# Optimization experiments

Measured on AMD Instinct MI355X. Metric: run time of the kernel, lower is better.

The kernel has to match this reference:

```python
import jax, jax.numpy as jnp
import numpy as np

K = 16          # neighbors per point
POINTNUM = 2048 # opt.pointnum
B, N = 8, 2048


def _knn_concat(x, k):
    """x: [B,N,C] -> [B,N,k,2C] = concat(center, k-nearest neighbor feats)."""
    sq = jnp.sum(x * x, axis=-1)                                   # [B,N]
    d2 = sq[:, :, None] + sq[:, None, :] - 2.0 * jnp.einsum('bnc,bmc->bnm', x, x)
    _, idx = jax.lax.top_k(-d2, k)                                 # [B,N,k]
    nbr = jax.vmap(lambda xb, ib: xb[ib])(x, idx)                  # [B,N,k,C]
    ctr = jnp.broadcast_to(x[:, :, None, :], nbr.shape)
    return jnp.concatenate([ctr, nbr], axis=-1)


def _lin(x, w, b):
    return x @ w + b


lrelu = jax.nn.leaky_relu  # default negative_slope=0.01 matches nn.LeakyReLU()


def setup_inputs() -> dict:
    key = jax.random.key(0)
    ks = jax.random.split(key, 20)

    def w(k_, fi, fo):
        return jax.random.normal(k_, (fi, fo), jnp.float32) / np.sqrt(fi)

    inp = {
        'x': jax.random.normal(ks[0], (B, N, 3), jnp.float32),
        'h1w1': w(ks[1], 6, 16),   'h1b1': jnp.zeros((16,), jnp.float32),
        'h1w2': w(ks[2], 16, 64),  'h1b2': jnp.zeros((64,), jnp.float32),
        'h1w3': w(ks[3], 64, 32),  'h1b3': jnp.zeros((32,), jnp.float32),
        'h2w1': w(ks[4], 64, 256), 'h2b1': jnp.zeros((256,), jnp.float32),
        'h2w2': w(ks[5], 256, 128),'h2b2': jnp.zeros((128,), jnp.float32),
        'h3w1': w(ks[6], 256, 128),'h3b1': jnp.zeros((128,), jnp.float32),
        'fc1w': w(ks[7], 128, 128),'fc1b': jnp.zeros((128,), jnp.float32),
        'fc2w': w(ks[8], 128, 128),'fc2b': jnp.zeros((128,), jnp.float32),
        'fc3w': w(ks[9], 128, POINTNUM * 3), 'fc3b': jnp.zeros((POINTNUM * 3,), jnp.float32),
    }
    return inp


def reference(x, h1w1, h1b1, h1w2, h1b2, h1w3, h1b3,
              h2w1, h2b1, h2w2, h2b2, h3w1, h3b1,
              fc1w, fc1b, fc2w, fc2b, fc3w, fc3b):
    # block 1: knn-concat [B,N,K,6] -> MLP(6,16,64,32) -> sum over K
    x1 = _knn_concat(x, K)
    h = lrelu(_lin(x1, h1w1, h1b1))
    h = lrelu(_lin(h, h1w2, h1b2))
    h = lrelu(_lin(h, h1w3, h1b3))
    x2 = jnp.sum(h, axis=2)                    # [B,N,32]
    # block 2: [B,N,K,64] -> MLP(64,256,128) -> sum over K
    x2 = _knn_concat(x2, K)
    h = lrelu(_lin(x2, h2w1, h2b1))
    h = lrelu(_lin(h, h2w2, h2b2))
    x3 = jnp.sum(h, axis=2)                    # [B,N,128]
    # block 3: [B,N,K,256] -> MLP(256,128) -> sum over K
    x3 = _knn_concat(x3, K)
    h = lrelu(_lin(x3, h3w1, h3b1))
    x4 = jnp.sum(h, axis=2)                    # [B,N,128]
    # global max pool over points
    x5 = jnp.max(x4, axis=1)                   # [B,128]
    x6 = lrelu(_lin(x5, fc1w, fc1b))
    x7 = lrelu(_lin(x6, fc2w, fc2b))
    x8 = _lin(x7, fc3w, fc3b)                  # [B, POINTNUM*3]
    return x8.reshape(x8.shape[0], POINTNUM, 3)
```

## Files before the change

kernel.cpp:

```cpp
#include <hip/hip_runtime.h>

#define KNB 16
#define BSZ 8
#define NPT 2048

typedef __attribute__((ext_vector_type(8))) short bf16x8;
typedef __attribute__((ext_vector_type(4))) float f32x4;

__device__ __forceinline__ float lrelu(float x) { return x >= 0.f ? x : 0.01f * x; }

__device__ __forceinline__ unsigned short bf16rne(float f) {
    union { float f; unsigned int u; } v; v.f = f;
    return (unsigned short)((v.u + 0x7FFFu + ((v.u >> 16) & 1u)) >> 16);
}

__device__ __forceinline__ float packkey(float d, int idx) {
    union { float f; unsigned int u; } v; v.f = d;
    v.u = (v.u & 0xFFFFF800u) | (unsigned int)idx;
    return v.f;
}

__device__ __forceinline__ void ceA(float& a, float& b) {
    const float lo = fminf(a, b), hi = fmaxf(a, b);
    a = lo; b = hi;
}

__device__ __forceinline__ void bsort16(float* c) {
#pragma unroll
    for (int k = 2; k <= 16; k <<= 1) {
#pragma unroll
        for (int j = k >> 1; j > 0; j >>= 1) {
#pragma unroll
            for (int i = 0; i < 16; ++i) {
                const int l = i ^ j;
                if (l > i) {
                    if ((i & k) == 0) ceA(c[i], c[l]);
                    else              ceA(c[l], c[i]);
                }
            }
        }
    }
}

__device__ __forceinline__ void merge16(float* L, const float* C) {
#pragma unroll
    for (int i = 0; i < 16; ++i) L[i] = fminf(L[i], C[15 - i]);
#pragma unroll
    for (int j = 8; j > 0; j >>= 1) {
#pragma unroll
        for (int i = 0; i < 16; ++i) {
            const int l = i ^ j;
            if (l > i) ceA(L[i], L[l]);
        }
    }
}

__device__ __forceinline__ void st16(float* dst, const float* L) {
#pragma unroll
    for (int c = 0; c < 4; ++c)
        *(f32x4*)(dst + c * 4) = (f32x4){L[c * 4], L[c * 4 + 1], L[c * 4 + 2], L[c * 4 + 3]};
}

__device__ __forceinline__ void ld16(float* L, const float* src) {
#pragma unroll
    for (int c = 0; c < 4; ++c) {
        const f32x4 v = *(const f32x4*)(src + c * 4);
        L[c * 4] = v[0]; L[c * 4 + 1] = v[1]; L[c * 4 + 2] = v[2]; L[c * 4 + 3] = v[3];
    }
}

__device__ __forceinline__ void xwave_merge_out(float (*sS)[20], int w, int lane,
                                                float* L, float* outp) {
    st16(sS[w * 64 + lane], L);
    __syncthreads();
    if ((w & 1) == 0) {
        float C[16];
        ld16(C, sS[(w + 1) * 64 + lane]);
        merge16(L, C);
        if (w == 2) st16(sS[2 * 64 + lane], L);
    }
    __syncthreads();
    if (w == 0) {
        float C[16];
        ld16(C, sS[2 * 64 + lane]);
        merge16(L, C);
        st16(outp, L);
    }
}

__global__ void wprep_all_kernel(const float* __restrict__ h2w1, unsigned short* __restrict__ w1t,
                                 const float* __restrict__ h2w2, unsigned short* __restrict__ w2t,
                                 const float* __restrict__ h3w1, unsigned short* __restrict__ w3t,
                                 const float* __restrict__ w1, const float* __restrict__ w2,
                                 const float* __restrict__ w3,
                                 unsigned short* __restrict__ w1a, unsigned short* __restrict__ w2a,
                                 unsigned short* __restrict__ w3a) {
    const int bid = blockIdx.x, tid = threadIdx.x;
    if (bid < 64) {
        int i = bid * 256 + tid;
        int k = i >> 8, n = i & 255;
        w1t[n * 64 + k] = bf16rne(h2w1[i]);
    } else if (bid < 192) {
        int i = (bid - 64) * 256 + tid;
        int k = i >> 7, n = i & 127;
        w2t[n * 256 + k] = bf16rne(h2w2[i]);
    } else if (bid < 320) {
        int i = (bid - 192) * 256 + tid;
        int k = i >> 7, n = i & 127;
        w3t[n * 256 + k] = bf16rne(h3w1[i]);
    } else {
        int i = (bid - 320) * 256 + tid;
        if (i < 512) {
            int n = i >> 5, k = i & 31;
            w1a[i] = (k < 6) ? bf16rne(w1[k * 16 + n]) : (unsigned short)0;
        } else if (i < 2560) {
            int j = i - 512, n = j >> 5, k = j & 31;
            w2a[j] = (k < 16) ? bf16rne(w2[k * 64 + n]) : (unsigned short)0;
        } else if (i < 4608) {
            int j = i - 2560, n = j >> 6, k = j & 63;
            w3a[j] = bf16rne(w3[k * 32 + n]);
        }
    }
}

template<int C>
__global__ void norms_kernel(const float* __restrict__ feat, float* __restrict__ out) {
    int gid = blockIdx.x * blockDim.x + threadIdx.x;
    if (gid < BSZ * NPT) {
        const float* p = feat + (size_t)gid * C;
        float s = 0.f;
#pragma unroll
        for (int c = 0; c < C; ++c) s = fmaf(p[c], p[c], s);
        out[gid] = s;
    }
}

__global__ void norms16q_kernel(const unsigned short* __restrict__ feat, float* __restrict__ out) {
    const int gid = blockIdx.x * 256 + threadIdx.x;
    const int q = gid >> 2, prt = gid & 3;
    const unsigned short* p = feat + (size_t)q * 128 + prt * 32;
    float s = 0.f;
#pragma unroll
    for (int c8 = 0; c8 < 4; ++c8) {
        const bf16x8 v = *(const bf16x8*)(p + c8 * 8);
#pragma unroll
        for (int j = 0; j < 8; ++j) {
            union { unsigned int u; float f; } t;
            t.u = ((unsigned int)(unsigned short)v[j]) << 16;
            s = fmaf(t.f, t.f, s);
        }
    }
    s += __shfl_xor(s, 1);
    s += __shfl_xor(s, 2);
    if (prt == 0) out[q] = s;
}

template<int JS>
__launch_bounds__(256, 3)
__global__ void knn3_kernel(const float* __restrict__ feat,
                            const float* __restrict__ norms,
                            float* __restrict__ cand) {
    constexpr int JL = NPT / JS;
    constexpr int JP = JL / 4;
    const int b = blockIdx.z, js = blockIdx.y, i0 = blockIdx.x * 64;
    const int t = threadIdx.x, w = t >> 6, lane = t & 63;
    const float* fb = feat + (size_t)b * NPT * 3;
    const float* nb = norms + (size_t)b * NPT;

    __shared__ __align__(16) float sS[256][20];

    float q0, q1, q2;
    { const float* qp = fb + (size_t)(i0 + lane) * 3; q0 = qp[0]; q1 = qp[1]; q2 = qp[2]; }

    float L[16];
#pragma unroll
    for (int u = 0; u < 16; ++u) L[u] = 3e38f;

    const int jbeg = js * JL + w * JP;
#pragma unroll 1
    for (int j0 = jbeg; j0 < jbeg + JP; j0 += 16) {
        float C[16];
#pragma unroll
        for (int u = 0; u < 16; ++u) {
            const int j = j0 + u;
            const float* pp = fb + (size_t)j * 3;
            C[u] = packkey(fmaf(-2.f, fmaf(q0, pp[0], fmaf(q1, pp[1], q2 * pp[2])), nb[j]), j);
        }
        bsort16(C);
        merge16(L, C);
    }
    float* o = cand + (((size_t)b * NPT + i0 + lane) * JS + js) * 16;
    xwave_merge_out(sS, w, lane, L, o);
}

template<int C, int JS>
__launch_bounds__(256, 3)
__global__ void knn_mfma_kernel(const unsigned short* __restrict__ fb16,
                                const float* __restrict__ norms,
                                float* __restrict__ cand) {
    constexpr int JL = NPT / JS;
    constexpr int KS = C / 32;
    const int b    = blockIdx.z;
    const int js   = blockIdx.y;
    const int i0   = blockIdx.x * 64;
    const int t    = threadIdx.x;
    const int w    = t >> 6;
    const int lane = t & 63;
    const int l15  = lane & 15;
    const int quad = lane >> 4;
    const unsigned short* fbb = fb16 + (size_t)b * NPT * C;
    const float* nb = norms + (size_t)b * NPT;

    __shared__ __align__(16) float sS[256][20];

    bf16x8 afr[KS * 4];
#pragma unroll
    for (int ks = 0; ks < KS; ++ks)
#pragma unroll
        for (int mi = 0; mi < 4; ++mi)
            afr[ks * 4 + mi] = *(const bf16x8*)(fbb + (size_t)(i0 + mi * 16 + l15) * C + ks * 32 + quad * 8);

    float L[16];
#pragma unroll
    for (int u = 0; u < 16; ++u) L[u] = 3e38f;

    const int jbeg = js * JL;
#pragma unroll 1
    for (int j0 = jbeg; j0 < jbeg + JL; j0 += 64) {
        f32x4 acc[4];
#pragma unroll
        for (int mi = 0; mi < 4; ++mi) acc[mi] = (f32x4){0.f, 0.f, 0.f, 0.f};
        const unsigned short* prow = fbb + (size_t)(j0 + w * 16 + l15) * C + quad * 8;
#pragma unroll
        for (int ks = 0; ks < KS; ++ks) {
            const bf16x8 bfr = *(const bf16x8*)(prow + ks * 32);
#pragma unroll
            for (int mi = 0; mi < 4; ++mi)
                acc[mi] = __builtin_amdgcn_mfma_f32_16x16x32_bf16(afr[ks * 4 + mi], bfr, acc[mi], 0, 0, 0);
        }
        const float nv  = nb[j0 + w * 16 + l15];
        const int  cidx = j0 + w * 16 + l15;
#pragma unroll
        for (int mi = 0; mi < 4; ++mi)
#pragma unroll
            for (int r = 0; r < 4; ++r)
                sS[w * 64 + mi * 16 + quad * 4 + r][l15] = packkey(fmaf(-2.f, acc[mi][r], nv), cidx);
        float Cb[16];
        ld16(Cb, sS[w * 64 + lane]);
        bsort16(Cb);
        merge16(L, Cb);
    }

    float* o = cand + (((size_t)b * NPT + i0 + lane) * JS + js) * 16;
    xwave_merge_out(sS, w, lane, L, o);
}

template<int JS>
__launch_bounds__(64)
__global__ void knn_merge_kernel(const float* __restrict__ cand, int* __restrict__ knn_out) {
    const int q = blockIdx.x * 64 + threadIdx.x;
    const float* pd = cand + (size_t)q * JS * 16;
    float L[16];
    ld16(L, pd);
#pragma unroll
    for (int s = 1; s < JS; ++s) {
        float C[16];
        ld16(C, pd + s * 16);
        merge16(L, C);
    }
    int* o = knn_out + (size_t)q * KNB;
#pragma unroll
    for (int u = 0; u < 16; ++u) {
        union { float f; unsigned int v; } z; z.f = L[u];
        o[u] = (int)(z.v & 2047u);
    }
}

__launch_bounds__(256, 3)
__global__ void block1_mfma_kernel(const float* __restrict__ x, const int* __restrict__ knn,
                                   const unsigned short* __restrict__ w1a, const float* __restrict__ b1,
                                   const unsigned short* __restrict__ w2a, const float* __restrict__ b2,
                                   const unsigned short* __restrict__ w3a, const float* __restrict__ b3,
                                   unsigned short* __restrict__ x2b, float* __restrict__ nrm) {
    const int w = threadIdx.x >> 6, lane = threadIdx.x & 63;
    const int l15 = lane & 15, quad = lane >> 4;

    const bf16x8 W1 = *(const bf16x8*)(w1a + l15 * 32 + quad * 8);
    bf16x8 W2[4];
#pragma unroll
    for (int nt = 0; nt < 4; ++nt)
        W2[nt] = *(const bf16x8*)(w2a + (nt * 16 + l15) * 32 + quad * 8);
    bf16x8 W3[2][2];
#pragma unroll
    for (int tt = 0; tt < 2; ++tt)
#pragma unroll
        for (int ks = 0; ks < 2; ++ks)
            W3[tt][ks] = *(const bf16x8*)(w3a + (tt * 16 + l15) * 64 + ks * 32 + quad * 8);
    float b1v[4], b2v[4][4], b3v[2][4];
#pragma unroll
    for (int r = 0; r < 4; ++r) b1v[r] = b1[quad * 4 + r];
#pragma unroll
    for (int nt = 0; nt < 4; ++nt)
#pragma unroll
        for (int r = 0; r < 4; ++r) b2v[nt][r] = b2[nt * 16 + quad * 4 + r];
#pragma unroll
    for (int tt = 0; tt < 2; ++tt)
#pragma unroll
        for (int r = 0; r < 4; ++r) b3v[tt][r] = b3[tt * 16 + quad * 4 + r];

    const int src0 = ((2 * quad) & 3) * 16 + l15;
    const int src1 = ((2 * quad + 1) & 3) * 16 + l15;
    const int ntsel = quad >> 1;

    const int p0 = blockIdx.x * 8 + w * 2;
#pragma unroll 2
    for (int pi = 0; pi < 2; ++pi) {
        const int p = p0 + pi, b = p >> 11, n = p & (NPT - 1);
        int d0 = 0, d1 = 0, d2 = 0;
        if (quad == 0) {
            const float* xc = x + ((size_t)b * NPT + n) * 3;
            const int jn = knn[(size_t)p * KNB + l15];
            const float* xn = x + ((size_t)b * NPT + jn) * 3;
            const unsigned s0 = bf16rne(xc[0]), s1 = bf16rne(xc[1]), s2 = bf16rne(xc[2]);
            const unsigned s3 = bf16rne(xn[0]), s4 = bf16rne(xn[1]), s5 = bf16rne(xn[2]);
            d0 = (int)(s0 | (s1 << 16));
            d1 = (int)(s2 | (s3 << 16));
            d2 = (int)(s4 | (s5 << 16));
        }
        union { int i[4]; bf16x8 v; } B1;
        B1.i[0] = d0; B1.i[1] = d1; B1.i[2] = d2; B1.i[3] = 0;
        const f32x4 a1 = __builtin_amdgcn_mfma_f32_16x16x32_bf16(W1, B1.v, (f32x4){0.f, 0.f, 0.f, 0.f}, 0, 0, 0);

        int h10, h11;
        {
            const unsigned t0 = bf16rne(lrelu(a1[0] + b1v[0]));
            const unsigned t1 = bf16rne(lrelu(a1[1] + b1v[1]));
            const unsigned t2 = bf16rne(lrelu(a1[2] + b1v[2]));
            const unsigned t3 = bf16rne(lrelu(a1[3] + b1v[3]));
            h10 = (int)(t0 | (t1 << 16));
            h11 = (int)(t2 | (t3 << 16));
        }
        union { int i[4]; bf16x8 v; } B2;
        {
            const int e0 = __shfl(h10, src0), e1 = __shfl(h11, src0);
            const int e2 = __shfl(h10, src1), e3 = __shfl(h11, src1);
            const bool val = quad < 2;
            B2.i[0] = val ? e0 : 0; B2.i[1] = val ? e1 : 0;
            B2.i[2] = val ? e2 : 0; B2.i[3] = val ? e3 : 0;
        }
        f32x4 a2[4];
#pragma unroll
        for (int nt = 0; nt < 4; ++nt)
            a2[nt] = __builtin_amdgcn_mfma_f32_16x16x32_bf16(W2[nt], B2.v, (f32x4){0.f, 0.f, 0.f, 0.f}, 0, 0, 0);
        int dpk[4][2];
#pragma unroll
        for (int nt = 0; nt < 4; ++nt) {
            const unsigned t0 = bf16rne(lrelu(a2[nt][0] + b2v[nt][0]));
            const unsigned t1 = bf16rne(lrelu(a2[nt][1] + b2v[nt][1]));
            const unsigned t2 = bf16rne(lrelu(a2[nt][2] + b2v[nt][2]));
            const unsigned t3 = bf16rne(lrelu(a2[nt][3] + b2v[nt][3]));
            dpk[nt][0] = (int)(t0 | (t1 << 16));
            dpk[nt][1] = (int)(t2 | (t3 << 16));
        }
        f32x4 a3[2] = { (f32x4){0.f, 0.f, 0.f, 0.f}, (f32x4){0.f, 0.f, 0.f, 0.f} };
#pragma unroll
        for (int ks = 0; ks < 2; ++ks) {
            union { int i[4]; bf16x8 v; } B3;
            const int a0l = __shfl(dpk[2 * ks][0], src0), a0h = __shfl(dpk[2 * ks + 1][0], src0);
            const int a1l = __shfl(dpk[2 * ks][1], src0), a1h = __shfl(dpk[2 * ks + 1][1], src0);
            const int a2l = __shfl(dpk[2 * ks][0], src1), a2h = __shfl(dpk[2 * ks + 1][0], src1);
            const int a3l = __shfl(dpk[2 * ks][1], src1), a3h = __shfl(dpk[2 * ks + 1][1], src1);
            B3.i[0] = ntsel ? a0h : a0l;
            B3.i[1] = ntsel ? a1h : a1l;
            B3.i[2] = ntsel ? a2h : a2l;
            B3.i[3] = ntsel ? a3h : a3l;
#pragma unroll
            for (int tt = 0; tt < 2; ++tt)
                a3[tt] = __builtin_amdgcn_mfma_f32_16x16x32_bf16(W3[tt][ks], B3.v, a3[tt], 0, 0, 0);
        }
        float na = 0.f;
#pragma unroll
        for (int tt = 0; tt < 2; ++tt) {
#pragma unroll
            for (int r = 0; r < 4; ++r) {
                float s = lrelu(a3[tt][r] + b3v[tt][r]);
                s += __shfl_xor(s, 1);
                s += __shfl_xor(s, 2);
                s += __shfl_xor(s, 4);
                s += __shfl_xor(s, 8);
                na = fmaf(s, s, na);
                if (l15 == 0)
                    x2b[(size_t)p * 32 + tt * 16 + quad * 4 + r] = bf16rne(s);
            }
        }
        na += __shfl_xor(na, 16);
        na += __shfl_xor(na, 32);
        if (lane == 0) nrm[p] = na;
    }
}

__launch_bounds__(256, 2)
__global__ void block2_fused_kernel(const unsigned short* __restrict__ x2b,
                                    const int* __restrict__ knn,
                                    const unsigned short* __restrict__ w1t,
                                    const float* __restrict__ b1,
                                    const unsigned short* __restrict__ w2t,
                                    const float* __restrict__ b2,
                                    unsigned short* __restrict__ x3b) {
    const int w    = threadIdx.x >> 6;
    const int lane = threadIdx.x & 63;
    const int l15  = lane & 15, quad = lane >> 4;
    __shared__ __align__(16) unsigned short sH1[2][16][264];

    bf16x8 B1[4][2];
#pragma unroll
    for (int nt2 = 0; nt2 < 4; ++nt2)
#pragma unroll
        for (int ks = 0; ks < 2; ++ks)
            B1[nt2][ks] = *(const bf16x8*)(w1t + (size_t)(w * 64 + nt2 * 16 + l15) * 64 + ks * 32 + quad * 8);
    bf16x8 B2[2][8];
#pragma unroll
    for (int nt2 = 0; nt2 < 2; ++nt2)
#pragma unroll
        for (int ks = 0; ks < 8; ++ks)
            B2[nt2][ks] = *(const bf16x8*)(w2t + (size_t)(w * 32 + nt2 * 16 + l15) * 256 + ks * 32 + quad * 8);
    float b1v[4];
#pragma unroll
    for (int nt2 = 0; nt2 < 4; ++nt2) b1v[nt2] = b1[w * 64 + nt2 * 16 + l15];
    float b2v[2];
#pragma unroll
    for (int nt2 = 0; nt2 < 2; ++nt2) b2v[nt2] = b2[w * 32 + nt2 * 16 + l15];

    const int p0 = blockIdx.x * 8;
#pragma unroll 1
    for (int pi = 0; pi < 8; ++pi) {
        const int p = p0 + pi, b = p >> 11, buf = pi & 1;
        const int nbr = knn[(size_t)p * KNB + l15];
        const bf16x8 a0 = *(const bf16x8*)(x2b + (size_t)p * 32 + quad * 8);
        const bf16x8 a1 = *(const bf16x8*)(x2b + ((size_t)(b * NPT) + nbr) * 32 + quad * 8);
#pragma unroll
        for (int nt2 = 0; nt2 < 4; ++nt2) {
            f32x4 acc = (f32x4){0.f, 0.f, 0.f, 0.f};
            acc = __builtin_amdgcn_mfma_f32_16x16x32_bf16(a0, B1[nt2][0], acc, 0, 0, 0);
            acc = __builtin_amdgcn_mfma_f32_16x16x32_bf16(a1, B1[nt2][1], acc, 0, 0, 0);
#pragma unroll
            for (int r = 0; r < 4; ++r)
                sH1[buf][quad * 4 + r][w * 64 + nt2 * 16 + l15] = bf16rne(lrelu(acc[r] + b1v[nt2]));
        }
        __syncthreads();
        bf16x8 af[8];
#pragma unroll
        for (int ks = 0; ks < 8; ++ks)
            af[ks] = *(const bf16x8*)&sH1[buf][l15][ks * 32 + quad * 8];
#pragma unroll
        for (int nt2 = 0; nt2 < 2; ++nt2) {
            f32x4 acc = (f32x4){0.f, 0.f, 0.f, 0.f};
#pragma unroll
            for (int ks = 0; ks < 8; ++ks)
                acc = __builtin_amdgcn_mfma_f32_16x16x32_bf16(af[ks], B2[nt2][ks], acc, 0, 0, 0);
            float s = 0.f;
#pragma unroll
            for (int r = 0; r < 4; ++r) s += lrelu(acc[r] + b2v[nt2]);
            s += __shfl_xor(s, 16);
            s += __shfl_xor(s, 32);
            if (quad == 0) x3b[(size_t)p * 128 + w * 32 + nt2 * 16 + l15] = bf16rne(s);
        }
    }
}

__launch_bounds__(256, 3)
__global__ void block3_fused_kernel(const unsigned short* __restrict__ x3b,
                                    const int* __restrict__ knn,
                                    const unsigned short* __restrict__ w3t,
                                    const float* __restrict__ bias,
                                    float* __restrict__ x4) {
    const int w    = threadIdx.x >> 6;
    const int lane = threadIdx.x & 63;
    const int l15  = lane & 15, quad = lane >> 4;

    bf16x8 B3[2][8];
#pragma unroll
    for (int nt2 = 0; nt2 < 2; ++nt2)
#pragma unroll
        for (int ks = 0; ks < 8; ++ks)
            B3[nt2][ks] = *(const bf16x8*)(w3t + (size_t)(w * 32 + nt2 * 16 + l15) * 256 + ks * 32 + quad * 8);
    float bv[2];
#pragma unroll
    for (int nt2 = 0; nt2 < 2; ++nt2) bv[nt2] = bias[w * 32 + nt2 * 16 + l15];

    const int p0 = blockIdx.x * 8;
    const unsigned short* xb = x3b + (size_t)(p0 >> 11) * NPT * 128;

    int nbrv[8];
#pragma unroll
    for (int pi = 0; pi < 8; ++pi) nbrv[pi] = knn[(size_t)(p0 + pi) * KNB + l15];

    auto LDAF = [&](bf16x8* af, int pi, int nbr) {
        const unsigned short* ctr = x3b + (size_t)(p0 + pi) * 128 + quad * 8;
        const unsigned short* nbp = xb + (size_t)nbr * 128 + quad * 8;
#pragma unroll
        for (int ks = 0; ks < 4; ++ks) af[ks] = *(const bf16x8*)(ctr + ks * 32);
#pragma unroll
        for (int ks = 0; ks < 4; ++ks) af[4 + ks] = *(const bf16x8*)(nbp + ks * 32);
    };
    auto CMP = [&](int p, const bf16x8* af) {
#pragma unroll
        for (int nt2 = 0; nt2 < 2; ++nt2) {
            f32x4 acc = (f32x4){0.f, 0.f, 0.f, 0.f};
#pragma unroll
            for (int ks = 0; ks < 8; ++ks)
                acc = __builtin_amdgcn_mfma_f32_16x16x32_bf16(af[ks], B3[nt2][ks], acc, 0, 0, 0);
            float s = 0.f;
#pragma unroll
            for (int r = 0; r < 4; ++r) s += lrelu(acc[r] + bv[nt2]);
            s += __shfl_xor(s, 16);
            s += __shfl_xor(s, 32);
            if (quad == 0) x4[(size_t)p * 128 + w * 32 + nt2 * 16 + l15] = s;
        }
    };

    bf16x8 afA[8], afB[8];
    LDAF(afA, 0, nbrv[0]);
#pragma unroll
    for (int pj = 0; pj < 4; ++pj) {
        LDAF(afB, 2 * pj + 1, nbrv[2 * pj + 1]);
        CMP(p0 + 2 * pj, afA);
        if (pj < 3) LDAF(afA, 2 * pj + 2, nbrv[2 * pj + 2]);
        CMP(p0 + 2 * pj + 1, afB);
    }
}

__launch_bounds__(128)
__global__ void maxpool_partial_kernel(const float* __restrict__ x4,
                                       float* __restrict__ part) {
    const int chunk = blockIdx.x, b = blockIdx.y, t = threadIdx.x;
    const float* xb = x4 + ((size_t)b * NPT + (size_t)chunk * 64) * 128;
    float m = -1e30f;
#pragma unroll 8
    for (int n = 0; n < 64; ++n) m = fmaxf(m, xb[(size_t)n * 128 + t]);
    part[((size_t)b * 32 + chunk) * 128 + t] = m;
}

__launch_bounds__(128)
__global__ void head2_kernel(const float* __restrict__ part,
                             const float* __restrict__ fc1w, const float* __restrict__ fc1b,
                             const float* __restrict__ fc2w, const float* __restrict__ fc2b,
                             const float* __restrict__ fc3w, const float* __restrict__ fc3b,
                             float* __restrict__ out) {
    const int g = blockIdx.x, b = blockIdx.y, t = threadIdx.x;
    __shared__ float s5[128], s6[128], s7[128];
    float m = -1e30f;
#pragma unroll
    for (int c = 0; c < 32; ++c)
        m = fmaxf(m, part[((size_t)b * 32 + c) * 128 + t]);
    s5[t] = m;
    __syncthreads();
    float a = fc1b[t];
#pragma unroll 4
    for (int i = 0; i < 128; ++i) a = fmaf(s5[i], fc1w[i * 128 + t], a);
    s6[t] = lrelu(a);
    __syncthreads();
    a = fc2b[t];
#pragma unroll 4
    for (int i = 0; i < 128; ++i) a = fmaf(s6[i], fc2w[i * 128 + t], a);
    s7[t] = lrelu(a);
    __syncthreads();
    const int o = g * 128 + t;
    float acc = fc3b[o];
#pragma unroll 4
    for (int i = 0; i < 128; ++i) acc = fmaf(s7[i], fc3w[(size_t)i * 6144 + o], acc);
    out[(size_t)b * 6144 + o] = acc;
}

extern "C" void kernel_launch(void* const* d_in, const int* in_sizes, int n_in,
                              void* d_out, int out_size, void* d_ws, size_t ws_size,
                              hipStream_t stream) {
    const float* x    = (const float*)d_in[0];
    const float* h1w1 = (const float*)d_in[1];
    const float* h1b1 = (const float*)d_in[2];
    const float* h1w2 = (const float*)d_in[3];
    const float* h1b2 = (const float*)d_in[4];
    const float* h1w3 = (const float*)d_in[5];
    const float* h1b3 = (const float*)d_in[6];
    const float* h2w1 = (const float*)d_in[7];
    const float* h2b1 = (const float*)d_in[8];
    const float* h2w2 = (const float*)d_in[9];
    const float* h2b2 = (const float*)d_in[10];
    const float* h3w1 = (const float*)d_in[11];
    const float* h3b1 = (const float*)d_in[12];
    const float* fc1w = (const float*)d_in[13];
    const float* fc1b = (const float*)d_in[14];
    const float* fc2w = (const float*)d_in[15];
    const float* fc2b = (const float*)d_in[16];
    const float* fc3w = (const float*)d_in[17];
    const float* fc3b = (const float*)d_in[18];

    float* ws = (float*)d_ws;
    unsigned short* x2b16 = (unsigned short*)ws;
    unsigned short* x3b16 = (unsigned short*)(ws + 262144);
    float* x4   = ws + 1310720;
    float* cd   = x4;
    int*   idx  = (int*)(ws + 3407872);
    float* nrm  = ws + 3670016;
    unsigned short* w1t = (unsigned short*)(ws + 3702784);
    unsigned short* w2t = (unsigned short*)(ws + 3710976);
    unsigned short* w3t = (unsigned short*)(ws + 3727360);
    unsigned short* w1a = (unsigned short*)(ws + 3743744);
    unsigned short* w2a = (unsigned short*)(ws + 3744000);
    unsigned short* w3a = (unsigned short*)(ws + 3745024);
    float* part = ws + 3746048;
    float* out  = (float*)d_out;

    const dim3 kg(32, 8, 8);

    wprep_all_kernel<<<338, 256, 0, stream>>>(h2w1, w1t, h2w2, w2t, h3w1, w3t,
                                              h1w1, h1w2, h1w3, w1a, w2a, w3a);

    norms_kernel<3><<<64, 256, 0, stream>>>(x, nrm);
    knn3_kernel<8><<<kg, 256, 0, stream>>>(x, nrm, cd);
    knn_merge_kernel<8><<<256, 64, 0, stream>>>(cd, idx);
    block1_mfma_kernel<<<2048, 256, 0, stream>>>(x, idx, w1a, h1b1, w2a, h1b2, w3a, h1b3,
                                                 x2b16, nrm);

    knn_mfma_kernel<32, 8><<<kg, 256, 0, stream>>>(x2b16, nrm, cd);
    knn_merge_kernel<8><<<256, 64, 0, stream>>>(cd, idx);
    block2_fused_kernel<<<BSZ * NPT / 8, 256, 0, stream>>>(x2b16, idx, w1t, h2b1, w2t, h2b2, x3b16);

    norms16q_kernel<<<256, 256, 0, stream>>>(x3b16, nrm);
    knn_mfma_kernel<128, 8><<<kg, 256, 0, stream>>>(x3b16, nrm, cd);
    knn_merge_kernel<8><<<256, 64, 0, stream>>>(cd, idx);
    block3_fused_kernel<<<BSZ * NPT / 8, 256, 0, stream>>>(x3b16, idx, w3t, h3b1, x4);

    maxpool_partial_kernel<<<dim3(32, 8), 128, 0, stream>>>(x4, part);
    head2_kernel<<<dim3(48, 8), 128, 0, stream>>>(part, fc1w, fc1b, fc2w, fc2b,
                                                  fc3w, fc3b, out);
}
```

Measured before the change: 364.5 us.

## Widen block2/block3 to 8 waves, raise kNN occupancy, seed top-k from first chunk

Block2 and block3 fused kernels now use 512-thread blocks of 8 waves. Each wave owns 16 output columns instead of 32, which halves the per-wave weight fragments held in registers, and each block processes 16 points. The kNN kernels raise their launch-bound occupancy hint and fill the running top-16 list directly from the first sorted chunk, skipping one merge. The aim is more resident waves and fewer registers per wave. The cost is that block3 loses its explicit load/compute double-buffering, and more waves contend for the same syncthreads.

```diff
diff --git a/kernel.cpp b/kernel.cpp
--- a/kernel.cpp
+++ b/kernel.cpp
@@ -156,7 +156,7 @@
 }
 
 template<int JS>
-__launch_bounds__(256, 3)
+__launch_bounds__(256, 4)
 __global__ void knn3_kernel(const float* __restrict__ feat,
                             const float* __restrict__ norms,
                             float* __restrict__ cand) {
@@ -173,9 +173,6 @@
     { const float* qp = fb + (size_t)(i0 + lane) * 3; q0 = qp[0]; q1 = qp[1]; q2 = qp[2]; }
 
     float L[16];
-#pragma unroll
-    for (int u = 0; u < 16; ++u) L[u] = 3e38f;
-
     const int jbeg = js * JL + w * JP;
 #pragma unroll 1
     for (int j0 = jbeg; j0 < jbeg + JP; j0 += 16) {
@@ -187,14 +184,19 @@
             C[u] = packkey(fmaf(-2.f, fmaf(q0, pp[0], fmaf(q1, pp[1], q2 * pp[2])), nb[j]), j);
         }
         bsort16(C);
-        merge16(L, C);
+        if (j0 == jbeg) {
+#pragma unroll
+            for (int u = 0; u < 16; ++u) L[u] = C[u];
+        } else {
+            merge16(L, C);
+        }
     }
     float* o = cand + (((size_t)b * NPT + i0 + lane) * JS + js) * 16;
     xwave_merge_out(sS, w, lane, L, o);
 }
 
 template<int C, int JS>
-__launch_bounds__(256, 3)
+__launch_bounds__(256, C == 32 ? 4 : 3)
 __global__ void knn_mfma_kernel(const unsigned short* __restrict__ fb16,
                                 const float* __restrict__ norms,
                                 float* __restrict__ cand) {
@@ -221,9 +223,6 @@
             afr[ks * 4 + mi] = *(const bf16x8*)(fbb + (size_t)(i0 + mi * 16 + l15) * C + ks * 32 + quad * 8);
 
     float L[16];
-#pragma unroll
-    for (int u = 0; u < 16; ++u) L[u] = 3e38f;
-
     const int jbeg = js * JL;
 #pragma unroll 1
     for (int j0 = jbeg; j0 < jbeg + JL; j0 += 64) {
@@ -248,7 +247,12 @@
         float Cb[16];
         ld16(Cb, sS[w * 64 + lane]);
         bsort16(Cb);
-        merge16(L, Cb);
+        if (j0 == jbeg) {
+#pragma unroll
+            for (int u = 0; u < 16; ++u) L[u] = Cb[u];
+        } else {
+            merge16(L, Cb);
+        }
     }
 
     float* o = cand + (((size_t)b * NPT + i0 + lane) * JS + js) * 16;
@@ -399,7 +403,7 @@
     }
 }
 
-__launch_bounds__(256, 2)
+__launch_bounds__(512, 4)
 __global__ void block2_fused_kernel(const unsigned short* __restrict__ x2b,
                                     const int* __restrict__ knn,
                                     const unsigned short* __restrict__ w1t,
@@ -412,63 +416,63 @@
     const int l15  = lane & 15, quad = lane >> 4;
     __shared__ __align__(16) unsigned short sH1[2][16][264];
 
-    bf16x8 B1[4][2];
-#pragma unroll
-    for (int nt2 = 0; nt2 < 4; ++nt2)
+    bf16x8 B1[2][2];
+#pragma unroll
+    for (int nt2 = 0; nt2 < 2; ++nt2)
 #pragma unroll
         for (int ks = 0; ks < 2; ++ks)
-            B1[nt2][ks] = *(const bf16x8*)(w1t + (size_t)(w * 64 + nt2 * 16 + l15) * 64 + ks * 32 + quad * 8);
-    bf16x8 B2[2][8];
-#pragma unroll
-    for (int nt2 = 0; nt2 < 2; ++nt2)
-#pragma unroll
-        for (int ks = 0; ks < 8; ++ks)
-            B2[nt2][ks] = *(const bf16x8*)(w2t + (size_t)(w * 32 + nt2 * 16 + l15) * 256 + ks * 32 + quad * 8);
-    float b1v[4];
-#pragma unroll
-    for (int nt2 = 0; nt2 < 4; ++nt2) b1v[nt2] = b1[w * 64 + nt2 * 16 + l15];
-    float b2v[2];
-#pragma unroll
-    for (int nt2 = 0; nt2 < 2; ++nt2) b2v[nt2] = b2[w * 32 + nt2 * 16 + l15];
-
-    const int p0 = blockIdx.x * 8;
+            B1[nt2][ks] = *(const bf16x8*)(w1t + (size_t)(w * 32 + nt2 * 16 + l15) * 64 + ks * 32 + quad * 8);
+    bf16x8 B2[8];
+#pragma unroll
+    for (int ks = 0; ks < 8; ++ks)
+        B2[ks] = *(const bf16x8*)(w2t + (size_t)(w * 16 + l15) * 256 + ks * 32 + quad * 8);
+    float b1v[2];
+#pragma unroll
+    for (int nt2 = 0; nt2 < 2; ++nt2) b1v[nt2] = b1[w * 32 + nt2 * 16 + l15];
+    const float b2v = b2[w * 16 + l15];
+
+    const int p0 = blockIdx.x * 16;
+    const unsigned short* xb = x2b + (size_t)(p0 >> 11) * NPT * 32;
+
 #pragma unroll 1
-    for (int pi = 0; pi < 8; ++pi) {
-        const int p = p0 + pi, b = p >> 11, buf = pi & 1;
+    for (int pi = 0; pi < 16; ++pi) {
+        const int p = p0 + pi, buf = pi & 1;
         const int nbr = knn[(size_t)p * KNB + l15];
         const bf16x8 a0 = *(const bf16x8*)(x2b + (size_t)p * 32 + quad * 8);
-        const bf16x8 a1 = *(const bf16x8*)(x2b + ((size_t)(b * NPT) + nbr) * 32 + quad * 8);
-#pragma unroll
-        for (int nt2 = 0; nt2 < 4; ++nt2) {
+        const bf16x8 a1 = *(const bf16x8*)(xb + (size_t)nbr * 32 + quad * 8);
+#pragma unroll
+        for (int nt2 = 0; nt2 < 2; ++nt2) {
             f32x4 acc = (f32x4){0.f, 0.f, 0.f, 0.f};
             acc = __builtin_amdgcn_mfma_f32_16x16x32_bf16(a0, B1[nt2][0], acc, 0, 0, 0);
             acc = __builtin_amdgcn_mfma_f32_16x16x32_bf16(a1, B1[nt2][1], acc, 0, 0, 0);
 #pragma unroll
             for (int r = 0; r < 4; ++r)
-                sH1[buf][quad * 4 + r][w * 64 + nt2 * 16 + l15] = bf16rne(lrelu(acc[r] + b1v[nt2]));
+                sH1[buf][quad * 4 + r][w * 32 + nt2 * 16 + l15] = bf16rne(lrelu(acc[r] + b1v[nt2]));
         }
         __syncthreads();
-        bf16x8 af[8];
-#pragma unroll
-        for (int ks = 0; ks < 8; ++ks)
-            af[ks] = *(const bf16x8*)&sH1[buf][l15][ks * 32 + quad * 8];
-#pragma unroll
-        for (int nt2 = 0; nt2 < 2; ++nt2) {
-            f32x4 acc = (f32x4){0.f, 0.f, 0.f, 0.f};
-#pragma unroll
-            for (int ks = 0; ks < 8; ++ks)
-                acc = __builtin_amdgcn_mfma_f32_16x16x32_bf16(af[ks], B2[nt2][ks], acc, 0, 0, 0);
-            float s = 0.f;
-#pragma unroll
-            for (int r = 0; r < 4; ++r) s += lrelu(acc[r] + b2v[nt2]);
-            s += __shfl_xor(s, 16);
-            s += __shfl_xor(s, 32);
-            if (quad == 0) x3b[(size_t)p * 128 + w * 32 + nt2 * 16 + l15] = bf16rne(s);
-        }
-    }
-}
-
-__launch_bounds__(256, 3)
+        bf16x8 afA[4], afB[4];
+#pragma unroll
+        for (int ks = 0; ks < 4; ++ks)
+            afA[ks] = *(const bf16x8*)&sH1[buf][l15][ks * 32 + quad * 8];
+#pragma unroll
+        for (int ks = 0; ks < 4; ++ks)
+            afB[ks] = *(const bf16x8*)&sH1[buf][l15][128 + ks * 32 + quad * 8];
+        f32x4 accA = (f32x4){0.f, 0.f, 0.f, 0.f}, accB = (f32x4){0.f, 0.f, 0.f, 0.f};
+#pragma unroll
+        for (int ks = 0; ks < 4; ++ks) {
+            accA = __builtin_amdgcn_mfma_f32_16x16x32_bf16(afA[ks], B2[ks], accA, 0, 0, 0);
+            accB = __builtin_amdgcn_mfma_f32_16x16x32_bf16(afB[ks], B2[4 + ks], accB, 0, 0, 0);
+        }
+        float s = 0.f;
+#pragma unroll
+        for (int r = 0; r < 4; ++r) s += lrelu(accA[r] + accB[r] + b2v);
+        s += __shfl_xor(s, 16);
+        s += __shfl_xor(s, 32);
+        if (quad == 0) x3b[(size_t)p * 128 + w * 16 + l15] = bf16rne(s);
+    }
+}
+
+__launch_bounds__(512, 4)
 __global__ void block3_fused_kernel(const unsigned short* __restrict__ x3b,
                                     const int* __restrict__ knn,
                                     const unsigned short* __restrict__ w3t,
@@ -478,55 +482,38 @@
     const int lane = threadIdx.x & 63;
     const int l15  = lane & 15, quad = lane >> 4;
 
-    bf16x8 B3[2][8];
-#pragma unroll
-    for (int nt2 = 0; nt2 < 2; ++nt2)
-#pragma unroll
-        for (int ks = 0; ks < 8; ++ks)
-            B3[nt2][ks] = *(const bf16x8*)(w3t + (size_t)(w * 32 + nt2 * 16 + l15) * 256 + ks * 32 + quad * 8);
-    float bv[2];
-#pragma unroll
-    for (int nt2 = 0; nt2 < 2; ++nt2) bv[nt2] = bias[w * 32 + nt2 * 16 + l15];
-
-    const int p0 = blockIdx.x * 8;
+    bf16x8 B3[8];
+#pragma unroll
+    for (int ks = 0; ks < 8; ++ks)
+        B3[ks] = *(const bf16x8*)(w3t + (size_t)(w * 16 + l15) * 256 + ks * 32 + quad * 8);
+    const float bv = bias[w * 16 + l15];
+
+    const int p0 = blockIdx.x * 16;
     const unsigned short* xb = x3b + (size_t)(p0 >> 11) * NPT * 128;
 
-    int nbrv[8];
-#pragma unroll
-    for (int pi = 0; pi < 8; ++pi) nbrv[pi] = knn[(size_t)(p0 + pi) * KNB + l15];
-
-    auto LDAF = [&](bf16x8* af, int pi, int nbr) {
-        const unsigned short* ctr = x3b + (size_t)(p0 + pi) * 128 + quad * 8;
+#pragma unroll 2
+    for (int pi = 0; pi < 16; ++pi) {
+        const int p = p0 + pi;
+        const int nbr = knn[(size_t)p * KNB + l15];
+        const unsigned short* ctr = x3b + (size_t)p * 128 + quad * 8;
         const unsigned short* nbp = xb + (size_t)nbr * 128 + quad * 8;
-#pragma unroll
-        for (int ks = 0; ks < 4; ++ks) af[ks] = *(const bf16x8*)(ctr + ks * 32);
-#pragma unroll
-        for (int ks = 0; ks < 4; ++ks) af[4 + ks] = *(const bf16x8*)(nbp + ks * 32);
-    };
-    auto CMP = [&](int p, const bf16x8* af) {
-#pragma unroll
-        for (int nt2 = 0; nt2 < 2; ++nt2) {
-            f32x4 acc = (f32x4){0.f, 0.f, 0.f, 0.f};
-#pragma unroll
-            for (int ks = 0; ks < 8; ++ks)
-                acc = __builtin_amdgcn_mfma_f32_16x16x32_bf16(af[ks], B3[nt2][ks], acc, 0, 0, 0);
-            float s = 0.f;
-#pragma unroll
-            for (int r = 0; r < 4; ++r) s += lrelu(acc[r] + bv[nt2]);
-            s += __shfl_xor(s, 16);
-            s += __shfl_xor(s, 32);
-            if (quad == 0) x4[(size_t)p * 128 + w * 32 + nt2 * 16 + l15] = s;
-        }
-    };
-
-    bf16x8 afA[8], afB[8];
-    LDAF(afA, 0, nbrv[0]);
-#pragma unroll
-    for (int pj = 0; pj < 4; ++pj) {
-        LDAF(afB, 2 * pj + 1, nbrv[2 * pj + 1]);
-        CMP(p0 + 2 * pj, afA);
-        if (pj < 3) LDAF(afA, 2 * pj + 2, nbrv[2 * pj + 2]);
-        CMP(p0 + 2 * pj + 1, afB);
+        bf16x8 afA[4], afB[4];
+#pragma unroll
+        for (int ks = 0; ks < 4; ++ks) afA[ks] = *(const bf16x8*)(ctr + ks * 32);
+#pragma unroll
+        for (int ks = 0; ks < 4; ++ks) afB[ks] = *(const bf16x8*)(nbp + ks * 32);
+        f32x4 accA = (f32x4){0.f, 0.f, 0.f, 0.f}, accB = (f32x4){0.f, 0.f, 0.f, 0.f};
+#pragma unroll
+        for (int ks = 0; ks < 4; ++ks) {
+            accA = __builtin_amdgcn_mfma_f32_16x16x32_bf16(afA[ks], B3[ks], accA, 0, 0, 0);
+            accB = __builtin_amdgcn_mfma_f32_16x16x32_bf16(afB[ks], B3[4 + ks], accB, 0, 0, 0);
+        }
+        float s = 0.f;
+#pragma unroll
+        for (int r = 0; r < 4; ++r) s += lrelu(accA[r] + accB[r] + bv);
+        s += __shfl_xor(s, 16);
+        s += __shfl_xor(s, 32);
+        if (quad == 0) x4[(size_t)p * 128 + w * 16 + l15] = s;
     }
 }
 
@@ -624,12 +611,12 @@
 
     knn_mfma_kernel<32, 8><<<kg, 256, 0, stream>>>(x2b16, nrm, cd);
     knn_merge_kernel<8><<<256, 64, 0, stream>>>(cd, idx);
-    block2_fused_kernel<<<BSZ * NPT / 8, 256, 0, stream>>>(x2b16, idx, w1t, h2b1, w2t, h2b2, x3b16);
+    block2_fused_kernel<<<BSZ * NPT / 16, 512, 0, stream>>>(x2b16, idx, w1t, h2b1, w2t, h2b2, x3b16);
 
     norms16q_kernel<<<256, 256, 0, stream>>>(x3b16, nrm);
     knn_mfma_kernel<128, 8><<<kg, 256, 0, stream>>>(x3b16, nrm, cd);
     knn_merge_kernel<8><<<256, 64, 0, stream>>>(cd, idx);
-    block3_fused_kernel<<<BSZ * NPT / 8, 256, 0, stream>>>(x3b16, idx, w3t, h3b1, x4);
+    block3_fused_kernel<<<BSZ * NPT / 16, 512, 0, stream>>>(x3b16, idx, w3t, h3b1, x4);
 
     maxpool_partial_kernel<<<dim3(32, 8), 128, 0, stream>>>(x4, part);
     head2_kernel<<<dim3(48, 8), 128, 0, stream>>>(part, fc1w, fc1b, fc2w, fc2b,
```

Measured after the change: 388.9 us. 6.7% more time.
